# Optimization experiments

Measured on AMD Instinct MI355X. Metric: run time of the kernel, lower is better.

## Reference

```python
import jax, jax.numpy as jnp
import numpy as np

C = 256
SQ = C // 4  # squeeze_channels

def hardsigmoid(v):
    # torch Hardsigmoid: relu6(v + 3) / 6
    return jnp.clip(v / 6.0 + 0.5, 0.0, 1.0)

def setup_inputs() -> dict:
    key = jax.random.key(0)
    k1, k2, k3, k4, k5 = jax.random.split(key, 5)
    x = jax.random.normal(k1, (32, C, 64, 64), dtype=jnp.float32)
    # Conv2d 1x1 weights stored as [out, in] (kernel dims squeezed)
    s1 = 1.0 / np.sqrt(C)
    s2 = 1.0 / np.sqrt(SQ)
    W1 = jax.random.uniform(k2, (SQ, C), jnp.float32, -s1, s1)
    b1 = jax.random.uniform(k3, (SQ,), jnp.float32, -s1, s1)
    W2 = jax.random.uniform(k4, (C, SQ), jnp.float32, -s2, s2)
    b2 = jax.random.uniform(k5, (C,), jnp.float32, -s2, s2)
    return {"x": x, "W1": W1, "b1": b1, "W2": W2, "b2": b2}

def reference(x, W1, b1, W2, b2):
    # fc1 (1x1 conv) applied on full spatial map, then mean over (H, W)
    # scale: [B, SQ, H, W] -> mean -> [B, SQ]
    s = jnp.einsum('bchw,oc->bohw', x, W1) + b1[None, :, None, None]
    s = s.mean(axis=(2, 3))                      # [B, SQ]
    s = jax.nn.relu(s)
    s = jnp.einsum('bo,co->bc', s, W2) + b2      # [B, C]
    gate = hardsigmoid(s)[:, :, None, None]      # [B, C, 1, 1]
    return x * gate
```

## Files before the change

### kernel.cpp

```cpp
#include <hip/hip_runtime.h>


#define SE_B  32
#define SE_C  256
#define SE_SQ 64
#define SE_HW 4096
#define CPB   16
#define TPB   512
#define VPT   32
#define N_RE  5
#define N_LDS 7
#define N_REG 20
#define RDY_STRIDE 32

typedef float f32x4 __attribute__((ext_vector_type(4)));

__device__ __forceinline__ float hsig(float v) {
    return fminf(fmaxf(v * (1.0f / 6.0f) + 0.5f, 0.0f), 1.0f);
}

__global__ __launch_bounds__(TPB, 4) void se_fused_kernel(
    const float* __restrict__ x,
    const float* __restrict__ W1, const float* __restrict__ b1,
    const float* __restrict__ W2, const float* __restrict__ b2,
    float* __restrict__ m, int* __restrict__ ready,
    float* __restrict__ y) {
    const int blk  = blockIdx.x;
    const int b    = blk >> 4;
    const int c0   = (blk & 15) * CPB;
    const int t    = threadIdx.x;
    const int wave = t >> 6;
    const int lane = t & 63;

    __shared__ f32x4 ldsdata[N_LDS * TPB];
    __shared__ float partials[CPB * 8];
    __shared__ f32x4 m4_lds[SE_C / 4];
    __shared__ float s_lds[SE_SQ];
    __shared__ float g_lds[CPB];

    const size_t base = ((size_t)b * SE_C + c0) * (SE_HW / 4);
    const f32x4* xv = reinterpret_cast<const f32x4*>(x) + base;
    f32x4*       yv = reinterpret_cast<f32x4*>(y)       + base;

    f32x4 keep[N_REG];
    float part = 0.0f;
#pragma unroll
    for (int k = 0; k < VPT; ++k) {
        f32x4 v = xv[k * TPB + t];
        if (k >= N_RE && k < N_RE + N_LDS) ldsdata[(k - N_RE) * TPB + t] = v;
        if (k >= N_RE + N_LDS)             keep[k - (N_RE + N_LDS)] = v;
        part += (v.x + v.y) + (v.z + v.w);
        if (k & 1) {
            float p = part;
#pragma unroll
            for (int off = 1; off < 64; off <<= 1) p += __shfl_xor(p, off);
            if (lane == 0) partials[(k >> 1) * 8 + wave] = p;
            part = 0.0f;
        }
    }
    __syncthreads();

    if (t < CPB) {
        float s = 0.0f;
#pragma unroll
        for (int w = 0; w < 8; ++w) s += partials[t * 8 + w];
        m[b * SE_C + c0 + t] = s * (1.0f / SE_HW);
    }
    __syncthreads();

    if (t == 0) {
        __hip_atomic_fetch_add(&ready[b * RDY_STRIDE], 1,
                               __ATOMIC_RELEASE, __HIP_MEMORY_SCOPE_AGENT);
        while (__hip_atomic_load(&ready[b * RDY_STRIDE],
                                 __ATOMIC_ACQUIRE, __HIP_MEMORY_SCOPE_AGENT) < CPB)
            __builtin_amdgcn_s_sleep(2);
    }
    __syncthreads();

    if (t < SE_C / 4)
        m4_lds[t] = reinterpret_cast<const f32x4*>(m + b * SE_C)[t];
    __syncthreads();

    const f32x4* W1v = reinterpret_cast<const f32x4*>(W1);
    const f32x4 mv = m4_lds[lane];
#pragma unroll
    for (int i = 0; i < 8; ++i) {
        const int o = wave * 8 + i;
        f32x4 w4 = W1v[o * 64 + lane];
        float p = w4.x * mv.x;
        p = fmaf(w4.y, mv.y, p);
        p = fmaf(w4.z, mv.z, p);
        p = fmaf(w4.w, mv.w, p);
#pragma unroll
        for (int off = 1; off < 64; off <<= 1) p += __shfl_xor(p, off);
        if (lane == 0) s_lds[o] = fmaxf(p + b1[o], 0.0f);
    }
    __syncthreads();

#pragma unroll
    for (int i = 0; i < 2; ++i) {
        const int cl = wave * 2 + i;
        const int c  = c0 + cl;
        float p = W2[c * SE_SQ + lane] * s_lds[lane];
#pragma unroll
        for (int off = 1; off < 64; off <<= 1) p += __shfl_xor(p, off);
        if (lane == 0) g_lds[cl] = hsig(p + b2[c]);
    }
    __syncthreads();

#pragma unroll
    for (int k = 0; k < VPT; ++k) {
        const float g = g_lds[k >> 1];
        f32x4 v;
        if (k < N_RE)                 v = xv[k * TPB + t];
        else if (k < N_RE + N_LDS)    v = ldsdata[(k - N_RE) * TPB + t];
        else                          v = keep[k - (N_RE + N_LDS)];
        v *= g;
        __builtin_nontemporal_store(v, &yv[k * TPB + t]);
    }
}

extern "C" void kernel_launch(void* const* d_in, const int* in_sizes, int n_in,
                              void* d_out, int out_size, void* d_ws, size_t ws_size,
                              hipStream_t stream) {
    const float* x  = (const float*)d_in[0];
    const float* W1 = (const float*)d_in[1];
    const float* b1 = (const float*)d_in[2];
    const float* W2 = (const float*)d_in[3];
    const float* b2 = (const float*)d_in[4];
    float* y = (float*)d_out;

    float* m     = (float*)d_ws;
    int*   ready = (int*)(m + SE_B * SE_C);

    hipMemsetAsync(ready, 0, SE_B * RDY_STRIDE * sizeof(int), stream);
    se_fused_kernel<<<SE_B * (SE_C / CPB), TPB, 0, stream>>>(
        x, W1, b1, W2, b2, m, ready, y);
}
```

Baseline: 72.50 us.

## Rebalance register/LDS/reload split of x and reorder output phase

Changes which slices of x are kept on-chip between the mean pass and the scaling pass. Registers now hold 12 vectors instead of 20, LDS holds 9 instead of 7, and the re-read from global memory grows from 5 vectors to 11. The first pass keeps 16 independent partial accumulators and does all the cross-lane reductions after the loads. The output phase now issues the global re-reads first, then the LDS-held data, then the register-held data, so the global reads can overlap with the rest. The aim is lower register pressure and better overlap of memory traffic, at the cost of more LDS per block and more global re-reads.

```diff
diff --git a/kernel.cpp b/kernel.cpp
--- a/kernel.cpp
+++ b/kernel.cpp
@@ -8,9 +8,8 @@
 #define CPB   16
 #define TPB   512
 #define VPT   32
-#define N_RE  5
-#define N_LDS 7
-#define N_REG 20
+#define N_REG 12
+#define N_LDS 9
 #define RDY_STRIDE 32
 
 typedef float f32x4 __attribute__((ext_vector_type(4)));
@@ -32,7 +31,7 @@
     const int wave = t >> 6;
     const int lane = t & 63;
 
-    __shared__ f32x4 ldsdata[N_LDS * TPB];
+    __shared__ f32x4 lds[N_LDS * TPB];
     __shared__ float partials[CPB * 8];
     __shared__ f32x4 m4_lds[SE_C / 4];
     __shared__ float s_lds[SE_SQ];
@@ -42,20 +41,41 @@
     const f32x4* xv = reinterpret_cast<const f32x4*>(x) + base;
     f32x4*       yv = reinterpret_cast<f32x4*>(y)       + base;
 
-    f32x4 keep[N_REG];
-    float part = 0.0f;
+    f32x4 r0, r1, r2, r3, r4, r5, r6, r7, r8, r9, r10, r11;
+    float a0=0,a1=0,a2=0,a3=0,a4=0,a5=0,a6=0,a7=0,
+          a8=0,a9=0,a10=0,a11=0,a12=0,a13=0,a14=0,a15=0;
+
+#define SUM4(v) ((v.x + v.y) + (v.z + v.w))
+#define ST_REG(k, r, a)  { f32x4 v = xv[(k)*TPB + t]; r = v;                    a += SUM4(v); }
+#define ST_LDS(k, a)     { f32x4 v = xv[(k)*TPB + t]; lds[((k)-N_REG)*TPB+t]=v; a += SUM4(v); }
+#define ST_NONE(k, a)    { f32x4 v = xv[(k)*TPB + t];                           a += SUM4(v); }
+
+    ST_REG( 0, r0,  a0)  ST_REG( 1, r1,  a0)
+    ST_REG( 2, r2,  a1)  ST_REG( 3, r3,  a1)
+    ST_REG( 4, r4,  a2)  ST_REG( 5, r5,  a2)
+    ST_REG( 6, r6,  a3)  ST_REG( 7, r7,  a3)
+    ST_REG( 8, r8,  a4)  ST_REG( 9, r9,  a4)
+    ST_REG(10, r10, a5)  ST_REG(11, r11, a5)
+    ST_LDS(12, a6)  ST_LDS(13, a6)
+    ST_LDS(14, a7)  ST_LDS(15, a7)
+    ST_LDS(16, a8)  ST_LDS(17, a8)
+    ST_LDS(18, a9)  ST_LDS(19, a9)
+    ST_LDS(20, a10)
+    ST_NONE(21, a10)
+    ST_NONE(22, a11) ST_NONE(23, a11)
+    ST_NONE(24, a12) ST_NONE(25, a12)
+    ST_NONE(26, a13) ST_NONE(27, a13)
+    ST_NONE(28, a14) ST_NONE(29, a14)
+    ST_NONE(30, a15) ST_NONE(31, a15)
+
+    {
+        float acc[16] = {a0,a1,a2,a3,a4,a5,a6,a7,a8,a9,a10,a11,a12,a13,a14,a15};
 #pragma unroll
-    for (int k = 0; k < VPT; ++k) {
-        f32x4 v = xv[k * TPB + t];
-        if (k >= N_RE && k < N_RE + N_LDS) ldsdata[(k - N_RE) * TPB + t] = v;
-        if (k >= N_RE + N_LDS)             keep[k - (N_RE + N_LDS)] = v;
-        part += (v.x + v.y) + (v.z + v.w);
-        if (k & 1) {
-            float p = part;
+        for (int j = 0; j < 16; ++j) {
+            float p = acc[j];
 #pragma unroll
             for (int off = 1; off < 64; off <<= 1) p += __shfl_xor(p, off);
-            if (lane == 0) partials[(k >> 1) * 8 + wave] = p;
-            part = 0.0f;
+            if (lane == 0) partials[j * 8 + wave] = p;
         }
     }
     __syncthreads();
@@ -109,15 +129,22 @@
     __syncthreads();
 
 #pragma unroll
-    for (int k = 0; k < VPT; ++k) {
-        const float g = g_lds[k >> 1];
-        f32x4 v;
-        if (k < N_RE)                 v = xv[k * TPB + t];
-        else if (k < N_RE + N_LDS)    v = ldsdata[(k - N_RE) * TPB + t];
-        else                          v = keep[k - (N_RE + N_LDS)];
-        v *= g;
+    for (int k = N_REG + N_LDS; k < VPT; ++k) {
+        f32x4 v = xv[k * TPB + t];
+        v *= g_lds[k >> 1];
         __builtin_nontemporal_store(v, &yv[k * TPB + t]);
     }
+#pragma unroll
+    for (int k = N_REG; k < N_REG + N_LDS; ++k) {
+        f32x4 v = lds[(k - N_REG) * TPB + t];
+        v *= g_lds[k >> 1];
+        __builtin_nontemporal_store(v, &yv[k * TPB + t]);
+    }
+#define OUT_REG(k, r) { f32x4 v = r; v *= g_lds[(k) >> 1]; \
+                        __builtin_nontemporal_store(v, &yv[(k)*TPB + t]); }
+    OUT_REG( 0, r0)  OUT_REG( 1, r1)  OUT_REG( 2, r2)  OUT_REG( 3, r3)
+    OUT_REG( 4, r4)  OUT_REG( 5, r5)  OUT_REG( 6, r6)  OUT_REG( 7, r7)
+    OUT_REG( 8, r8)  OUT_REG( 9, r9)  OUT_REG(10, r10) OUT_REG(11, r11)
 }
 
 extern "C" void kernel_launch(void* const* d_in, const int* in_sizes, int n_in,
```

Result: slower. 105.8 us (+46.0%).

## Drop register stash, re-read most of x from global, keep more in LDS

Applied to the files above, without the earlier changes.

Stops holding 20 vectors per thread in registers and instead stages the first 9 vectors per thread in LDS while re-reading the remaining 23 from global (L2/MALL) in the scale phase. Per-channel partial sums are accumulated in 16 registers and reduced with wave shuffles only after all loads are issued, so the shuffle reductions no longer sit between loads. This is meant to cut register pressure and allow more loads in flight, at the cost of reading more of x from memory a second time and using more LDS per block, which may limit occupancy.

```diff
diff --git a/kernel.cpp b/kernel.cpp
--- a/kernel.cpp
+++ b/kernel.cpp
@@ -8,9 +8,7 @@
 #define CPB   16
 #define TPB   512
 #define VPT   32
-#define N_RE  5
-#define N_LDS 7
-#define N_REG 20
+#define N_LDS 9
 #define RDY_STRIDE 32
 
 typedef float f32x4 __attribute__((ext_vector_type(4)));
@@ -32,7 +30,7 @@
     const int wave = t >> 6;
     const int lane = t & 63;
 
-    __shared__ f32x4 ldsdata[N_LDS * TPB];
+    __shared__ f32x4 lds[N_LDS * TPB];
     __shared__ float partials[CPB * 8];
     __shared__ f32x4 m4_lds[SE_C / 4];
     __shared__ float s_lds[SE_SQ];
@@ -42,21 +40,20 @@
     const f32x4* xv = reinterpret_cast<const f32x4*>(x) + base;
     f32x4*       yv = reinterpret_cast<f32x4*>(y)       + base;
 
-    f32x4 keep[N_REG];
-    float part = 0.0f;
+    float acc[CPB] = {0};
 #pragma unroll
     for (int k = 0; k < VPT; ++k) {
         f32x4 v = xv[k * TPB + t];
-        if (k >= N_RE && k < N_RE + N_LDS) ldsdata[(k - N_RE) * TPB + t] = v;
-        if (k >= N_RE + N_LDS)             keep[k - (N_RE + N_LDS)] = v;
-        part += (v.x + v.y) + (v.z + v.w);
-        if (k & 1) {
-            float p = part;
+        if (k < N_LDS) lds[k * TPB + t] = v;
+        acc[k >> 1] += (v.x + v.y) + (v.z + v.w);
+    }
+
 #pragma unroll
-            for (int off = 1; off < 64; off <<= 1) p += __shfl_xor(p, off);
-            if (lane == 0) partials[(k >> 1) * 8 + wave] = p;
-            part = 0.0f;
-        }
+    for (int j = 0; j < CPB; ++j) {
+        float p = acc[j];
+#pragma unroll
+        for (int off = 1; off < 64; off <<= 1) p += __shfl_xor(p, off);
+        if (lane == 0) partials[j * 8 + wave] = p;
     }
     __syncthreads();
 
@@ -109,13 +106,15 @@
     __syncthreads();
 
 #pragma unroll
-    for (int k = 0; k < VPT; ++k) {
-        const float g = g_lds[k >> 1];
-        f32x4 v;
-        if (k < N_RE)                 v = xv[k * TPB + t];
-        else if (k < N_RE + N_LDS)    v = ldsdata[(k - N_RE) * TPB + t];
-        else                          v = keep[k - (N_RE + N_LDS)];
-        v *= g;
+    for (int k = N_LDS; k < VPT; ++k) {
+        f32x4 v = xv[k * TPB + t];
+        v *= g_lds[k >> 1];
+        __builtin_nontemporal_store(v, &yv[k * TPB + t]);
+    }
+#pragma unroll
+    for (int k = 0; k < N_LDS; ++k) {
+        f32x4 v = lds[k * TPB + t];
+        v *= g_lds[k >> 1];
         __builtin_nontemporal_store(v, &yv[k * TPB + t]);
     }
 }
```

Result: slower. 122.0 us (+68.2%).
